# Performance work log

Measured on AMD Instinct MI355X. Metric: run time of the kernel, lower is better.

## Reference

```python
import jax, jax.numpy as jnp
import numpy as np

DK, DV, NH = 512, 256, 8  # matches init_kwargs


def rel_to_abs(x):
    # x: (B, N, L, 2L-1) -> (B, N, L, L) via pad/reshape trick
    B, N, L, _ = x.shape
    x = jnp.pad(x, ((0, 0), (0, 0), (0, 0), (0, 1)))          # (B,N,L,2L)
    x = x.reshape(B, N, L * 2 * L)
    x = jnp.pad(x, ((0, 0), (0, 0), (0, L - 1)))
    x = x.reshape(B, N, L + 1, 2 * L - 1)
    return x[:, :, :L, L - 1:]


def relative_logits_1d(q, rel_k):
    # q: (B, nh, A, Wd, dkh); rel_k: (dkh, 2*Wd-1)
    B, nh, A, Wd, _ = q.shape
    rel = jnp.einsum('bnawc,cm->bnawm', q, rel_k)             # (B,nh,A,Wd,2Wd-1)
    rel = rel.reshape(B, nh * A, Wd, 2 * Wd - 1)
    rel = rel_to_abs(rel).reshape(B, nh, A, 1, Wd, Wd)
    return jnp.broadcast_to(rel, (B, nh, A, A, Wd, Wd))


def reference(x, w_qkv, w_conv, w_out, key_rel_h, key_rel_w):
    B, Cin, H, W = x.shape
    dkh, dvh = DK // NH, DV // NH
    L = H * W
    # 1x1 qkv projection (stride 1)
    qkv = jnp.einsum('bchw,oc->bohw', x, w_qkv)               # (B, 2dk+dv, H, W)
    q = qkv[:, :DK]
    k = qkv[:, DK:2 * DK]
    v = qkv[:, 2 * DK:]
    flat_q = q.reshape(B, NH, dkh, L) * (dkh ** -0.5)
    flat_k = k.reshape(B, NH, dkh, L)
    flat_v = v.reshape(B, NH, dvh, L)
    logits = jnp.einsum('bncs,bnct->bnst', flat_q, flat_k)     # (B,nh,L,L)
    # relative position logits (uses the already-scaled q, as in the torch code)
    qr = flat_q.reshape(B, NH, dkh, H, W).transpose(0, 1, 3, 4, 2)  # (B,nh,H,W,dkh)
    w_rel = relative_logits_1d(qr, key_rel_w)                  # (B,nh,H,H,W,W)
    h_rel = relative_logits_1d(qr.transpose(0, 1, 3, 2, 4), key_rel_h)  # (B,nh,W,W,H,H)
    h_rel = h_rel.transpose(0, 1, 2, 4, 3, 5).reshape(B, NH, L, L)
    w_rel = w_rel.transpose(0, 1, 4, 2, 5, 3).reshape(B, NH, L, L)
    logits = logits + h_rel + w_rel
    weights = jax.nn.softmax(logits, axis=-1)
    attn = jnp.einsum('bnst,bnct->bnsc', weights, flat_v)      # (B,nh,L,dvh)
    attn = attn.transpose(0, 1, 3, 2).reshape(B, DV, H, W)
    attn = jnp.einsum('bchw,oc->bohw', attn, w_out)            # 1x1 out_proj
    conv_out = jax.lax.conv_general_dilated(
        x, w_conv, window_strides=(1, 1), padding=[(1, 1), (1, 1)],
        dimension_numbers=('NCHW', 'OIHW', 'NCHW'))            # (B, out_c-dv, H, W)
    return jnp.concatenate([conv_out, attn], axis=1)


def setup_inputs() -> dict:
    key = jax.random.key(0)
    ks = jax.random.split(key, 6)
    H, W, Cin = 32, 32, 256
    return {
        'x': jax.random.normal(ks[0], (8, Cin, H, W), jnp.float32),
        'w_qkv': jax.random.normal(ks[1], (2 * DK + DV, Cin), jnp.float32) * 0.02,
        'w_conv': jax.random.normal(ks[2], (256, Cin, 3, 3), jnp.float32) * 0.02,
        'w_out': jax.random.normal(ks[3], (DV, DV), jnp.float32) * 0.02,
        'key_rel_h': DK ** -0.5 + jax.random.normal(ks[4], (DK // NH, 2 * H - 1), jnp.float32),
        'key_rel_w': DK ** -0.5 + jax.random.normal(ks[5], (DK // NH, 2 * W - 1), jnp.float32),
    }
```

## Files before the change

kernel.cpp:

```cpp
#include <hip/hip_runtime.h>
#include <cstddef>
#include <cstdint>

#define NB 8
#define CIN 256
#define LL 1024
#define DKC 512
#define DVC 256
#define XPSTRIDE 295936

typedef short short8 __attribute__((ext_vector_type(8)));
typedef float f32x4 __attribute__((ext_vector_type(4)));

__device__ __forceinline__ unsigned short f2bf(float f) {
  unsigned int u = __float_as_uint(f);
  u += 0x7fffu + ((u >> 16) & 1u);
  return (unsigned short)(u >> 16);
}
__device__ __forceinline__ float bf2f(unsigned short u) {
  return __uint_as_float(((unsigned int)u) << 16);
}

__global__ __launch_bounds__(256) void prep_all(
    const float* __restrict__ x, const float* __restrict__ wconv,
    const float* __restrict__ wqkv, const float* __restrict__ wout,
    const float* __restrict__ krh, const float* __restrict__ krw,
    unsigned short* __restrict__ xTp, unsigned short* __restrict__ wtap,
    unsigned short* __restrict__ wqbf, unsigned short* __restrict__ woutbf,
    unsigned short* __restrict__ relTh, unsigned short* __restrict__ relTw) {
  __shared__ float tile[64][65];
  const int bx = blockIdx.x;
  const int tid = threadIdx.x;
  if (bx < 128) {
    const int st = bx & 15;
    const int b = bx >> 4;
    const int s0 = st * 64;
    const int h0 = st * 2;
    for (int cc = 0; cc < 4; ++cc) {
      const int c0 = cc * 64;
      {
        const int row = tid >> 2;
        const int j0 = (tid & 3) * 16;
#pragma unroll
        for (int k = 0; k < 4; ++k)
          *(float4*)&tile[row][j0 + k * 4] =
              *(const float4*)(x + ((size_t)(b * CIN + c0 + row)) * LL + s0 + j0 + k * 4);
      }
      __syncthreads();
      {
        const int sl = tid >> 2;
        const int cb = (tid & 3) * 16;
        unsigned short buf[16];
#pragma unroll
        for (int m = 0; m < 16; ++m) buf[m] = f2bf(tile[cb + m][sl]);
        const int hp = h0 + (sl >> 5) + 1;
        const int wp = (sl & 31) + 1;
        unsigned short* dst = xTp + (size_t)b * XPSTRIDE + (hp * 34 + wp) * 256 + c0 + cb;
        *(uint4*)dst = *(uint4*)&buf[0];
        *(uint4*)(dst + 8) = *(uint4*)&buf[8];
      }
      __syncthreads();
    }
  } else if (bx < 1184) {
    const int idx = (bx - 128) * 256 + tid;
    const int b = idx / 33792;
    const int rem = idx - b * 33792;
    const int pos = rem >> 8, c = rem & 255;
    int hp, wp;
    if (pos < 34) { hp = 0; wp = pos; }
    else if (pos < 68) { hp = 33; wp = pos - 34; }
    else if (pos < 100) { hp = pos - 68 + 1; wp = 0; }
    else { hp = pos - 100 + 1; wp = 33; }
    xTp[(size_t)b * XPSTRIDE + (hp * 34 + wp) * 256 + c] = 0;
  } else {
    const int idx = (bx - 1184) * 256 + tid;
    if (idx < 589824) {
      const int tap = idx >> 16;
      const int rem = idx & 65535;
      wtap[idx] = f2bf(wconv[(size_t)rem * 9 + tap]);
    } else if (idx < 917504) {
      const int j = idx - 589824;
      const int o = j >> 8;
      const float sc = (o < DKC) ? 0.125f * 1.44269504088896f : 1.0f;
      wqbf[j] = f2bf(wqkv[j] * sc);
    } else if (idx < 983040) {
      const int j = idx - 917504;
      woutbf[j] = f2bf(wout[j]);
    } else {
      const int j = idx - 983040;
      const int tbl = j >> 12;
      const int rest = j & 4095;
      const int m = rest >> 6, c = rest & 63;
      const float* src = tbl ? krw : krh;
      unsigned short* dst = tbl ? relTw : relTh;
      const float v = (m < 63) ? src[c * 63 + m] : 0.f;
      dst[m * 64 + c] = f2bf(v);
    }
  }
}

__global__ __launch_bounds__(256) void qkv_mfma(
    const unsigned short* __restrict__ xTp, const unsigned short* __restrict__ wqbf,
    unsigned short* __restrict__ qbf, unsigned short* __restrict__ kbf,
    unsigned short* __restrict__ vbf) {
  __shared__ __align__(16) char smem[16640];
  unsigned short* as = (unsigned short*)smem;
  unsigned short* bs = (unsigned short*)(smem + 8192);
  float (*trans)[65] = (float(*)[65])smem;

  const int tid = threadIdx.x;
  const int lane = tid & 63, w = tid >> 6;
  const int n16 = lane & 15, quad = lane >> 4;
  const int ot = blockIdx.x;
  const int st = blockIdx.y;
  const int b = blockIdx.z;
  const int o0 = ot * 64;
  const int s0 = st * 64;
  const int h0 = st * 2;
  const int trow = tid >> 3, ck = tid & 7;

  const unsigned short* xb = xTp + (size_t)b * XPSTRIDE;
  const unsigned short* wt = wqbf + (size_t)o0 * 256;
  const int wpos = (trow & 31) + 1;

  f32x4 acc[4];
#pragma unroll
  for (int nt = 0; nt < 4; ++nt) acc[nt] = (f32x4){0.f, 0.f, 0.f, 0.f};

  uint4 ra0, ra1, rb0, rb1;
  {
    ra0 = *(const uint4*)(wt + (size_t)trow * 256 + ck * 8);
    ra1 = *(const uint4*)(wt + (size_t)(trow + 32) * 256 + ck * 8);
    rb0 = *(const uint4*)(xb + (size_t)((h0 + 1) * 34 + wpos) * 256 + ck * 8);
    rb1 = *(const uint4*)(xb + (size_t)((h0 + 2) * 34 + wpos) * 256 + ck * 8);
  }
#pragma unroll
  for (int kc = 0; kc < 4; ++kc) {
    __syncthreads();
    *(uint4*)&as[trow * 64 + ((ck ^ (trow & 7)) * 8)] = ra0;
    *(uint4*)&as[(trow + 32) * 64 + ((ck ^ (trow & 7)) * 8)] = ra1;
    *(uint4*)&bs[trow * 64 + ((ck ^ (trow & 7)) * 8)] = rb0;
    *(uint4*)&bs[(trow + 32) * 64 + ((ck ^ (trow & 7)) * 8)] = rb1;
    __syncthreads();
    if (kc < 3) {
      const int c0 = (kc + 1) * 64;
      ra0 = *(const uint4*)(wt + (size_t)trow * 256 + c0 + ck * 8);
      ra1 = *(const uint4*)(wt + (size_t)(trow + 32) * 256 + c0 + ck * 8);
      rb0 = *(const uint4*)(xb + (size_t)((h0 + 1) * 34 + wpos) * 256 + c0 + ck * 8);
      rb1 = *(const uint4*)(xb + (size_t)((h0 + 2) * 34 + wpos) * 256 + c0 + ck * 8);
    }
    short8 a0 = *(const short8*)&as[(w * 16 + n16) * 64 + ((quad ^ (n16 & 7)) * 8)];
    short8 a1 = *(const short8*)&as[(w * 16 + n16) * 64 + (((quad + 4) ^ (n16 & 7)) * 8)];
#pragma unroll
    for (int nt = 0; nt < 4; ++nt) {
      short8 b0 = *(const short8*)&bs[(nt * 16 + n16) * 64 + ((quad ^ (n16 & 7)) * 8)];
      short8 b1 = *(const short8*)&bs[(nt * 16 + n16) * 64 + (((quad + 4) ^ (n16 & 7)) * 8)];
      acc[nt] = __builtin_amdgcn_mfma_f32_16x16x32_bf16(a0, b0, acc[nt], 0, 0, 0);
      acc[nt] = __builtin_amdgcn_mfma_f32_16x16x32_bf16(a1, b1, acc[nt], 0, 0, 0);
    }
  }
  __syncthreads();
#pragma unroll
  for (int nt = 0; nt < 4; ++nt)
#pragma unroll
    for (int reg = 0; reg < 4; ++reg)
      trans[w * 16 + quad * 4 + reg][nt * 16 + n16] = acc[nt][reg];
  __syncthreads();
  const int sl = tid >> 2;
  const int cseg = (tid & 3) * 16;
  unsigned short buf[16];
  if (ot < 16) {
#pragma unroll
    for (int m = 0; m < 16; ++m) buf[m] = f2bf(trans[cseg + m][sl]);
    unsigned short* dst;
    int head;
    if (ot < 8) { dst = qbf; head = ot; }
    else { dst = kbf; head = ot - 8; }
    const size_t base = (((size_t)(b * 8 + head)) * LL + s0 + sl) * 64 + cseg;
    *(uint4*)(dst + base) = *(uint4*)&buf[0];
    *(uint4*)(dst + base + 8) = *(uint4*)&buf[8];
  } else {
#pragma unroll
    for (int m = 0; m < 16; ++m) buf[m] = f2bf(trans[sl][cseg + m]);
    unsigned short* dst = vbf + ((size_t)b * DVC + (ot - 16) * 64 + sl) * LL + s0 + cseg;
    *(uint4*)dst = *(uint4*)&buf[0];
    *(uint4*)(dst + 8) = *(uint4*)&buf[8];
  }
}

__global__ __launch_bounds__(256) void conv_mfma(
    const unsigned short* __restrict__ xTp, const unsigned short* __restrict__ wtap,
    float* __restrict__ out) {
  __shared__ __align__(16) unsigned short as[2][64 * 64];
  __shared__ __align__(16) unsigned short bs[2][64 * 64];
  const int tid = threadIdx.x;
  const int lane = tid & 63, w = tid >> 6;
  const int n16 = lane & 15, quad = lane >> 4;
  const int ot = blockIdx.x;
  const int st = blockIdx.y;
  const int b = blockIdx.z;
  const int s0 = st * 64;
  const int h0 = st * 2;
  const int trow = tid >> 3;
  const int ck = tid & 7;

  const unsigned short* xb = xTp + (size_t)b * XPSTRIDE;
  const unsigned short* wbase = wtap + (size_t)(ot * 64) * 256;

  f32x4 acc[4];
#pragma unroll
  for (int nt = 0; nt < 4; ++nt) acc[nt] = (f32x4){0.f, 0.f, 0.f, 0.f};

  uint4 ra0, ra1, rb0, rb1;
  auto loadtile = [&](int it) {
    const int tap = it >> 2;
    const int c0 = (it & 3) * 64;
    const int dh = tap / 3 - 1;
    const int dw = tap - (tap / 3) * 3 - 1;
    const unsigned short* wt = wbase + (size_t)tap * 65536;
    ra0 = *(const uint4*)(wt + (size_t)trow * 256 + c0 + ck * 8);
    ra1 = *(const uint4*)(wt + (size_t)(trow + 32) * 256 + c0 + ck * 8);
    const int wp = (trow & 31) + dw + 1;
    rb0 = *(const uint4*)(xb + (size_t)((h0 + dh + 1) * 34 + wp) * 256 + c0 + ck * 8);
    rb1 = *(const uint4*)(xb + (size_t)((h0 + dh + 2) * 34 + wp) * 256 + c0 + ck * 8);
  };
  auto stage = [&](int bufi) {
    *(uint4*)&as[bufi][trow * 64 + ((ck ^ (trow & 7)) * 8)] = ra0;
    *(uint4*)&as[bufi][(trow + 32) * 64 + ((ck ^ (trow & 7)) * 8)] = ra1;
    *(uint4*)&bs[bufi][trow * 64 + ((ck ^ (trow & 7)) * 8)] = rb0;
    *(uint4*)&bs[bufi][(trow + 32) * 64 + ((ck ^ (trow & 7)) * 8)] = rb1;
  };
  loadtile(0);
  stage(0);
  for (int it = 0; it < 36; ++it) {
    if (it < 35) loadtile(it + 1);
    __syncthreads();
    const unsigned short* ab = as[it & 1];
    const unsigned short* bb = bs[it & 1];
    short8 a0 = *(const short8*)&ab[(w * 16 + n16) * 64 + ((quad ^ (n16 & 7)) * 8)];
    short8 a1 = *(const short8*)&ab[(w * 16 + n16) * 64 + (((quad + 4) ^ (n16 & 7)) * 8)];
#pragma unroll
    for (int nt = 0; nt < 4; ++nt) {
      short8 b0 = *(const short8*)&bb[(nt * 16 + n16) * 64 + ((quad ^ (n16 & 7)) * 8)];
      short8 b1 = *(const short8*)&bb[(nt * 16 + n16) * 64 + (((quad + 4) ^ (n16 & 7)) * 8)];
      acc[nt] = __builtin_amdgcn_mfma_f32_16x16x32_bf16(a0, b0, acc[nt], 0, 0, 0);
      acc[nt] = __builtin_amdgcn_mfma_f32_16x16x32_bf16(a1, b1, acc[nt], 0, 0, 0);
    }
    if (it < 35) stage((it + 1) & 1);
  }
#pragma unroll
  for (int nt = 0; nt < 4; ++nt)
#pragma unroll
    for (int reg = 0; reg < 4; ++reg)
      out[((size_t)b * 512 + ot * 64 + w * 16 + quad * 4 + reg) * LL + s0 + nt * 16 + n16] =
          acc[nt][reg];
}

__global__ __launch_bounds__(256, 4) void attn_kernel(
    const unsigned short* __restrict__ qbf, const unsigned short* __restrict__ kbf,
    const unsigned short* __restrict__ vbf, const unsigned short* __restrict__ relTh,
    const unsigned short* __restrict__ relTw, unsigned short* __restrict__ abf) {
  __shared__ __align__(16) char smem[28672];
  unsigned short* ks = (unsigned short*)smem;
  unsigned short* vs = (unsigned short*)(smem + 8192);
  unsigned short* ps = (unsigned short*)(smem + 12288);
  unsigned short* rwtT = (unsigned short*)(smem + 20480);
  float* obuf = (float*)smem;

  const int tid = threadIdx.x;
  const int lane = tid & 63, w = tid >> 6;
  const int n16 = lane & 15, quad = lane >> 4;
  const int blk = blockIdx.x;
  const int bn = blk & 63, qb = blk >> 6;
  const int n = bn & 7, b = bn >> 3;
  const int s0 = qb * 64;
  const int aa = 2 * qb + (w >> 1);
  const int pb = (w & 1) * 16;

  const unsigned short* qbase = qbf + ((size_t)(b * 8 + n)) * LL * 64;
  const unsigned short* kbase = kbf + ((size_t)(b * 8 + n)) * LL * 64;
  const unsigned short* vbase = vbf + ((size_t)(b * 8 + n)) * 32 * LL;

  const int ck = tid & 7;
  const int trow = tid >> 3;

  uint4 pk0 = *(const uint4*)(kbase + trow * 64 + ck * 8);
  uint4 pk1 = *(const uint4*)(kbase + (trow + 32) * 64 + ck * 8);
  uint4 pv = *(const uint4*)(vbase + (size_t)trow * LL + ck * 8);

  {
    const int sT = (pb + n16) * 32 + aa;
    short8 ra0 = *(const short8*)(qbase + (size_t)sT * 64 + quad * 8);
    short8 ra1 = *(const short8*)(qbase + (size_t)sT * 64 + 32 + quad * 8);
#pragma unroll
    for (int tbl = 0; tbl < 2; ++tbl) {
      const unsigned short* rel = tbl ? relTh : relTw;
      f32x4 acc[4];
#pragma unroll
      for (int mt = 0; mt < 4; ++mt) acc[mt] = (f32x4){0.f, 0.f, 0.f, 0.f};
#pragma unroll
      for (int mt = 0; mt < 4; ++mt) {
        short8 b0 = *(const short8*)(rel + (mt * 16 + n16) * 64 + quad * 8);
        short8 b1 = *(const short8*)(rel + (mt * 16 + n16) * 64 + 32 + quad * 8);
        acc[mt] = __builtin_amdgcn_mfma_f32_16x16x32_bf16(ra0, b0, acc[mt], 0, 0, 0);
        acc[mt] = __builtin_amdgcn_mfma_f32_16x16x32_bf16(ra1, b1, acc[mt], 0, 0, 0);
      }
      if (tbl == 0) {
#pragma unroll
        for (int mt = 0; mt < 4; ++mt)
#pragma unroll
          for (int reg = 0; reg < 4; ++reg)
            rwtT[(mt * 16 + n16) * 64 +
                 ((w * 16 + quad * 4 + reg) ^ ((n16 & 7) * 8))] = f2bf(acc[mt][reg]);
      } else {
#pragma unroll
        for (int mt = 0; mt < 4; ++mt)
#pragma unroll
          for (int reg = 0; reg < 4; ++reg)
            ps[(w * 16 + quad * 4 + reg) * 64 + mt * 16 + n16] = f2bf(acc[mt][reg]);
      }
    }
  }
  short8 qf0 = *(const short8*)(qbase + (size_t)(s0 + w * 16 + n16) * 64 + quad * 8);
  short8 qf1 = *(const short8*)(qbase + (size_t)(s0 + w * 16 + n16) * 64 + 32 + quad * 8);
  __syncthreads();
  float rhreg[2][4];
#pragma unroll
  for (int tt1 = 0; tt1 < 2; ++tt1)
#pragma unroll
    for (int reg = 0; reg < 4; ++reg) {
      const int iL = quad * 4 + reg;
      rhreg[tt1][reg] = bf2f(ps[(w * 16 + iL) * 64 + tt1 * 16 + n16 + 31 - pb - iL]);
    }

  float lacc[4] = {0.f, 0.f, 0.f, 0.f};
  f32x4 oacc[2];
  oacc[0] = (f32x4){0.f, 0.f, 0.f, 0.f};
  oacc[1] = (f32x4){0.f, 0.f, 0.f, 0.f};

  unsigned short* psw = ps + w * 1024;
  const int rb = w * 16 + quad * 4;

  for (int kt64 = 0; kt64 < 16; ++kt64) {
    const int t0 = kt64 * 64;
    __syncthreads();
    *(uint4*)&ks[trow * 64 + ((ck ^ (trow & 7)) * 8)] = pk0;
    *(uint4*)&ks[(trow + 32) * 64 + ((ck ^ (trow & 7)) * 8)] = pk1;
    *(uint4*)&vs[trow * 64 + ((ck ^ (trow & 7)) * 8)] = pv;
    __syncthreads();
    if (kt64 < 15) {
      const unsigned short* kg = kbase + (size_t)(t0 + 64) * 64;
      pk0 = *(const uint4*)(kg + trow * 64 + ck * 8);
      pk1 = *(const uint4*)(kg + (trow + 32) * 64 + ck * 8);
      pv = *(const uint4*)(vbase + (size_t)trow * LL + t0 + 64 + ck * 8);
    }

    f32x4 sacc[4];
#pragma unroll
    for (int tt = 0; tt < 4; ++tt) sacc[tt] = (f32x4){0.f, 0.f, 0.f, 0.f};
#pragma unroll
    for (int tt = 0; tt < 4; ++tt) {
      short8 kb0 = *(const short8*)&ks[(tt * 16 + n16) * 64 + ((quad ^ (n16 & 7)) * 8)];
      short8 kb1 = *(const short8*)&ks[(tt * 16 + n16) * 64 + (((quad + 4) ^ (n16 & 7)) * 8)];
      sacc[tt] = __builtin_amdgcn_mfma_f32_16x16x32_bf16(qf0, kb0, sacc[tt], 0, 0, 0);
      sacc[tt] = __builtin_amdgcn_mfma_f32_16x16x32_bf16(qf1, kb1, sacc[tt], 0, 0, 0);
    }
    float rwv[2][4];
#pragma unroll
    for (int h = 0; h < 2; ++h) {
      const int mw = (t0 >> 5) + h - aa + 31;
      const ushort4 rw4 = *(const ushort4*)&rwtT[mw * 64 + (rb ^ ((mw & 7) * 8))];
      rwv[h][0] = bf2f(rw4.x); rwv[h][1] = bf2f(rw4.y);
      rwv[h][2] = bf2f(rw4.z); rwv[h][3] = bf2f(rw4.w);
    }
#pragma unroll
    for (int tt = 0; tt < 4; ++tt)
#pragma unroll
      for (int reg = 0; reg < 4; ++reg) {
        const float e =
            __builtin_amdgcn_exp2f(sacc[tt][reg] + rwv[tt >> 1][reg] + rhreg[tt & 1][reg]);
        lacc[reg] += e;
        const int r = quad * 4 + reg;
        psw[r * 64 + (((tt * 2 + (n16 >> 3)) ^ (r & 7)) * 8) + (n16 & 7)] =
            (unsigned short)(__float_as_uint(e) >> 16);
      }
    __asm__ volatile("s_waitcnt lgkmcnt(0)" ::: "memory");
#pragma unroll
    for (int kt = 0; kt < 2; ++kt) {
      short8 pa = *(const short8*)&psw[n16 * 64 + (((quad + 4 * kt) ^ (n16 & 7)) * 8)];
#pragma unroll
      for (int ct = 0; ct < 2; ++ct) {
        short8 vb = *(const short8*)&vs[(ct * 16 + n16) * 64 + (((quad + 4 * kt) ^ (n16 & 7)) * 8)];
        oacc[ct] = __builtin_amdgcn_mfma_f32_16x16x32_bf16(pa, vb, oacc[ct], 0, 0, 0);
      }
    }
  }
  float linv[4];
#pragma unroll
  for (int reg = 0; reg < 4; ++reg) {
    float l = lacc[reg];
#pragma unroll
    for (int m = 1; m < 16; m <<= 1) l += __shfl_xor(l, m, 16);
    linv[reg] = 1.0f / l;
  }
  __syncthreads();
#pragma unroll
  for (int ct = 0; ct < 2; ++ct)
#pragma unroll
    for (int reg = 0; reg < 4; ++reg)
      obuf[(w * 16 + quad * 4 + reg) * 33 + ct * 16 + n16] = oacc[ct][reg] * linv[reg];
  __syncthreads();
  {
    const int row = tid >> 2;
    const int cseg = (tid & 3) * 8;
    unsigned short buf8[8];
#pragma unroll
    for (int m = 0; m < 8; ++m) buf8[m] = f2bf(obuf[row * 33 + cseg + m]);
    *(uint4*)(abf + (((size_t)b * LL) + s0 + row) * 256 + n * 32 + cseg) = *(uint4*)&buf8[0];
  }
}

__global__ __launch_bounds__(256) void proj_mfma(
    const unsigned short* __restrict__ abf, const unsigned short* __restrict__ woutbf,
    float* __restrict__ out) {
  __shared__ __align__(16) unsigned short as[64 * 64];
  __shared__ __align__(16) unsigned short bs[64 * 64];
  const int tid = threadIdx.x;
  const int lane = tid & 63, w = tid >> 6;
  const int n16 = lane & 15, quad = lane >> 4;
  const int ot = blockIdx.x;
  const int st = blockIdx.y;
  const int b = blockIdx.z;
  const int o0 = ot * 64;
  const int s0 = st * 64;
  const int trow = tid >> 3, ck = tid & 7;

  const unsigned short* ab = abf + ((size_t)b * LL + s0) * 256;
  const unsigned short* wt = woutbf + (size_t)o0 * 256;

  f32x4 acc[4];
#pragma unroll
  for (int nt = 0; nt < 4; ++nt) acc[nt] = (f32x4){0.f, 0.f, 0.f, 0.f};

  uint4 ra0, ra1, rb0, rb1;
  ra0 = *(const uint4*)(wt + (size_t)trow * 256 + ck * 8);
  ra1 = *(const uint4*)(wt + (size_t)(trow + 32) * 256 + ck * 8);
  rb0 = *(const uint4*)(ab + (size_t)trow * 256 + ck * 8);
  rb1 = *(const uint4*)(ab + (size_t)(trow + 32) * 256 + ck * 8);
#pragma unroll
  for (int kc = 0; kc < 4; ++kc) {
    __syncthreads();
    *(uint4*)&as[trow * 64 + ((ck ^ (trow & 7)) * 8)] = ra0;
    *(uint4*)&as[(trow + 32) * 64 + ((ck ^ (trow & 7)) * 8)] = ra1;
    *(uint4*)&bs[trow * 64 + ((ck ^ (trow & 7)) * 8)] = rb0;
    *(uint4*)&bs[(trow + 32) * 64 + ((ck ^ (trow & 7)) * 8)] = rb1;
    __syncthreads();
    if (kc < 3) {
      const int c0 = (kc + 1) * 64;
      ra0 = *(const uint4*)(wt + (size_t)trow * 256 + c0 + ck * 8);
      ra1 = *(const uint4*)(wt + (size_t)(trow + 32) * 256 + c0 + ck * 8);
      rb0 = *(const uint4*)(ab + (size_t)trow * 256 + c0 + ck * 8);
      rb1 = *(const uint4*)(ab + (size_t)(trow + 32) * 256 + c0 + ck * 8);
    }
    short8 a0 = *(const short8*)&as[(w * 16 + n16) * 64 + ((quad ^ (n16 & 7)) * 8)];
    short8 a1 = *(const short8*)&as[(w * 16 + n16) * 64 + (((quad + 4) ^ (n16 & 7)) * 8)];
#pragma unroll
    for (int nt = 0; nt < 4; ++nt) {
      short8 b0 = *(const short8*)&bs[(nt * 16 + n16) * 64 + ((quad ^ (n16 & 7)) * 8)];
      short8 b1 = *(const short8*)&bs[(nt * 16 + n16) * 64 + (((quad + 4) ^ (n16 & 7)) * 8)];
      acc[nt] = __builtin_amdgcn_mfma_f32_16x16x32_bf16(a0, b0, acc[nt], 0, 0, 0);
      acc[nt] = __builtin_amdgcn_mfma_f32_16x16x32_bf16(a1, b1, acc[nt], 0, 0, 0);
    }
  }
#pragma unroll
  for (int nt = 0; nt < 4; ++nt)
#pragma unroll
    for (int reg = 0; reg < 4; ++reg)
      out[((size_t)b * 512 + 256 + o0 + w * 16 + quad * 4 + reg) * LL + s0 + nt * 16 + n16] =
          acc[nt][reg];
}

extern "C" void kernel_launch(void* const* d_in, const int* in_sizes, int n_in,
                              void* d_out, int out_size, void* d_ws, size_t ws_size,
                              hipStream_t stream) {
  const float* x     = (const float*)d_in[0];
  const float* wqkv  = (const float*)d_in[1];
  const float* wconv = (const float*)d_in[2];
  const float* wout  = (const float*)d_in[3];
  const float* krh   = (const float*)d_in[4];
  const float* krw   = (const float*)d_in[5];
  float* out = (float*)d_out;

  unsigned short* qbf = (unsigned short*)d_ws;
  unsigned short* kbf = qbf + (size_t)NB * 8 * LL * 64;
  unsigned short* vbf = kbf + (size_t)NB * 8 * LL * 64;
  unsigned short* abf = vbf + (size_t)NB * DVC * LL;
  unsigned short* relTh = abf + (size_t)NB * LL * DVC;
  unsigned short* relTw = relTh + 4096;
  unsigned short* xTp = relTw + 4096;
  unsigned short* wtap = xTp + (size_t)NB * XPSTRIDE;
  unsigned short* wqbf = wtap + 589824;
  unsigned short* woutbf = wqbf + 327680;

  prep_all<<<dim3(5056), 256, 0, stream>>>(x, wconv, wqkv, wout, krh, krw,
                                           xTp, wtap, wqbf, woutbf, relTh, relTw);
  qkv_mfma<<<dim3(20, 16, NB), 256, 0, stream>>>(xTp, wqbf, qbf, kbf, vbf);
  conv_mfma<<<dim3(4, 16, NB), 256, 0, stream>>>(xTp, wtap, out);
  attn_kernel<<<dim3(1024), 256, 0, stream>>>(qbf, kbf, vbf, relTh, relTw, abf);
  proj_mfma<<<dim3(4, 16, NB), 256, 0, stream>>>(abf, woutbf, out);
}
```

Baseline: 154.0 us.

## Double-buffer K/V tiles in attention and halve conv spatial tile

The attention kernel now double-buffers its K/V shared-memory tiles. The next tile is written into the alternate buffer after the PV MFMAs, which removes one of the two block barriers per key tile. The conv kernel's spatial tile shrinks from 64 to 32 positions (one image row), doubling the grid to improve occupancy on the many CUs. Shared memory per attention block grows to about 40KB, which may lower occupancy, and the rwtT write skips the unused 64th row.

```diff
diff --git a/kernel.cpp b/kernel.cpp
--- a/kernel.cpp
+++ b/kernel.cpp
@@ -192,26 +192,25 @@
     const unsigned short* __restrict__ xTp, const unsigned short* __restrict__ wtap,
     float* __restrict__ out) {
   __shared__ __align__(16) unsigned short as[2][64 * 64];
-  __shared__ __align__(16) unsigned short bs[2][64 * 64];
+  __shared__ __align__(16) unsigned short bs[2][32 * 64];
   const int tid = threadIdx.x;
   const int lane = tid & 63, w = tid >> 6;
   const int n16 = lane & 15, quad = lane >> 4;
   const int ot = blockIdx.x;
   const int st = blockIdx.y;
   const int b = blockIdx.z;
-  const int s0 = st * 64;
-  const int h0 = st * 2;
+  const int s0 = st * 32;
   const int trow = tid >> 3;
   const int ck = tid & 7;
 
   const unsigned short* xb = xTp + (size_t)b * XPSTRIDE;
   const unsigned short* wbase = wtap + (size_t)(ot * 64) * 256;
 
-  f32x4 acc[4];
-#pragma unroll
-  for (int nt = 0; nt < 4; ++nt) acc[nt] = (f32x4){0.f, 0.f, 0.f, 0.f};
-
-  uint4 ra0, ra1, rb0, rb1;
+  f32x4 acc[2];
+#pragma unroll
+  for (int nt = 0; nt < 2; ++nt) acc[nt] = (f32x4){0.f, 0.f, 0.f, 0.f};
+
+  uint4 ra0, ra1, rb0;
   auto loadtile = [&](int it) {
     const int tap = it >> 2;
     const int c0 = (it & 3) * 64;
@@ -220,15 +219,13 @@
     const unsigned short* wt = wbase + (size_t)tap * 65536;
     ra0 = *(const uint4*)(wt + (size_t)trow * 256 + c0 + ck * 8);
     ra1 = *(const uint4*)(wt + (size_t)(trow + 32) * 256 + c0 + ck * 8);
-    const int wp = (trow & 31) + dw + 1;
-    rb0 = *(const uint4*)(xb + (size_t)((h0 + dh + 1) * 34 + wp) * 256 + c0 + ck * 8);
-    rb1 = *(const uint4*)(xb + (size_t)((h0 + dh + 2) * 34 + wp) * 256 + c0 + ck * 8);
+    const int wp = trow + dw + 1;
+    rb0 = *(const uint4*)(xb + (size_t)((st + dh + 1) * 34 + wp) * 256 + c0 + ck * 8);
   };
   auto stage = [&](int bufi) {
     *(uint4*)&as[bufi][trow * 64 + ((ck ^ (trow & 7)) * 8)] = ra0;
     *(uint4*)&as[bufi][(trow + 32) * 64 + ((ck ^ (trow & 7)) * 8)] = ra1;
     *(uint4*)&bs[bufi][trow * 64 + ((ck ^ (trow & 7)) * 8)] = rb0;
-    *(uint4*)&bs[bufi][(trow + 32) * 64 + ((ck ^ (trow & 7)) * 8)] = rb1;
   };
   loadtile(0);
   stage(0);
@@ -240,7 +237,7 @@
     short8 a0 = *(const short8*)&ab[(w * 16 + n16) * 64 + ((quad ^ (n16 & 7)) * 8)];
     short8 a1 = *(const short8*)&ab[(w * 16 + n16) * 64 + (((quad + 4) ^ (n16 & 7)) * 8)];
 #pragma unroll
-    for (int nt = 0; nt < 4; ++nt) {
+    for (int nt = 0; nt < 2; ++nt) {
       short8 b0 = *(const short8*)&bb[(nt * 16 + n16) * 64 + ((quad ^ (n16 & 7)) * 8)];
       short8 b1 = *(const short8*)&bb[(nt * 16 + n16) * 64 + (((quad + 4) ^ (n16 & 7)) * 8)];
       acc[nt] = __builtin_amdgcn_mfma_f32_16x16x32_bf16(a0, b0, acc[nt], 0, 0, 0);
@@ -249,7 +246,7 @@
     if (it < 35) stage((it + 1) & 1);
   }
 #pragma unroll
-  for (int nt = 0; nt < 4; ++nt)
+  for (int nt = 0; nt < 2; ++nt)
 #pragma unroll
     for (int reg = 0; reg < 4; ++reg)
       out[((size_t)b * 512 + ot * 64 + w * 16 + quad * 4 + reg) * LL + s0 + nt * 16 + n16] =
@@ -260,11 +257,11 @@
     const unsigned short* __restrict__ qbf, const unsigned short* __restrict__ kbf,
     const unsigned short* __restrict__ vbf, const unsigned short* __restrict__ relTh,
     const unsigned short* __restrict__ relTw, unsigned short* __restrict__ abf) {
-  __shared__ __align__(16) char smem[28672];
+  __shared__ __align__(16) char smem[40832];
   unsigned short* ks = (unsigned short*)smem;
-  unsigned short* vs = (unsigned short*)(smem + 8192);
-  unsigned short* ps = (unsigned short*)(smem + 12288);
-  unsigned short* rwtT = (unsigned short*)(smem + 20480);
+  unsigned short* vs = (unsigned short*)(smem + 16384);
+  unsigned short* ps = (unsigned short*)(smem + 24576);
+  unsigned short* rwtT = (unsigned short*)(smem + 32768);
   float* obuf = (float*)smem;
 
   const int tid = threadIdx.x;
@@ -306,12 +303,15 @@
         acc[mt] = __builtin_amdgcn_mfma_f32_16x16x32_bf16(ra1, b1, acc[mt], 0, 0, 0);
       }
       if (tbl == 0) {
-#pragma unroll
-        for (int mt = 0; mt < 4; ++mt)
-#pragma unroll
-          for (int reg = 0; reg < 4; ++reg)
-            rwtT[(mt * 16 + n16) * 64 +
-                 ((w * 16 + quad * 4 + reg) ^ ((n16 & 7) * 8))] = f2bf(acc[mt][reg]);
+        if ((3 * 16 + n16) < 63 || n16 < 15) {
+#pragma unroll
+          for (int mt = 0; mt < 4; ++mt)
+            if (mt * 16 + n16 < 63)
+#pragma unroll
+              for (int reg = 0; reg < 4; ++reg)
+                rwtT[(mt * 16 + n16) * 64 +
+                     ((w * 16 + quad * 4 + reg) ^ ((n16 & 7) * 8))] = f2bf(acc[mt][reg]);
+        }
       } else {
 #pragma unroll
         for (int mt = 0; mt < 4; ++mt)
@@ -323,6 +323,11 @@
   }
   short8 qf0 = *(const short8*)(qbase + (size_t)(s0 + w * 16 + n16) * 64 + quad * 8);
   short8 qf1 = *(const short8*)(qbase + (size_t)(s0 + w * 16 + n16) * 64 + 32 + quad * 8);
+  {
+    *(uint4*)&ks[trow * 64 + ((ck ^ (trow & 7)) * 8)] = pk0;
+    *(uint4*)&ks[(trow + 32) * 64 + ((ck ^ (trow & 7)) * 8)] = pk1;
+    *(uint4*)&vs[trow * 64 + ((ck ^ (trow & 7)) * 8)] = pv;
+  }
   __syncthreads();
   float rhreg[2][4];
 #pragma unroll
@@ -341,27 +346,26 @@
   unsigned short* psw = ps + w * 1024;
   const int rb = w * 16 + quad * 4;
 
+  int cur = 0;
   for (int kt64 = 0; kt64 < 16; ++kt64) {
     const int t0 = kt64 * 64;
-    __syncthreads();
-    *(uint4*)&ks[trow * 64 + ((ck ^ (trow & 7)) * 8)] = pk0;
-    *(uint4*)&ks[(trow + 32) * 64 + ((ck ^ (trow & 7)) * 8)] = pk1;
-    *(uint4*)&vs[trow * 64 + ((ck ^ (trow & 7)) * 8)] = pv;
-    __syncthreads();
     if (kt64 < 15) {
       const unsigned short* kg = kbase + (size_t)(t0 + 64) * 64;
       pk0 = *(const uint4*)(kg + trow * 64 + ck * 8);
       pk1 = *(const uint4*)(kg + (trow + 32) * 64 + ck * 8);
       pv = *(const uint4*)(vbase + (size_t)trow * LL + t0 + 64 + ck * 8);
     }
+    __syncthreads();
+    const unsigned short* ksb = ks + cur * 4096;
+    const unsigned short* vsb = vs + cur * 2048;
 
     f32x4 sacc[4];
 #pragma unroll
     for (int tt = 0; tt < 4; ++tt) sacc[tt] = (f32x4){0.f, 0.f, 0.f, 0.f};
 #pragma unroll
     for (int tt = 0; tt < 4; ++tt) {
-      short8 kb0 = *(const short8*)&ks[(tt * 16 + n16) * 64 + ((quad ^ (n16 & 7)) * 8)];
-      short8 kb1 = *(const short8*)&ks[(tt * 16 + n16) * 64 + (((quad + 4) ^ (n16 & 7)) * 8)];
+      short8 kb0 = *(const short8*)&ksb[(tt * 16 + n16) * 64 + ((quad ^ (n16 & 7)) * 8)];
+      short8 kb1 = *(const short8*)&ksb[(tt * 16 + n16) * 64 + (((quad + 4) ^ (n16 & 7)) * 8)];
       sacc[tt] = __builtin_amdgcn_mfma_f32_16x16x32_bf16(qf0, kb0, sacc[tt], 0, 0, 0);
       sacc[tt] = __builtin_amdgcn_mfma_f32_16x16x32_bf16(qf1, kb1, sacc[tt], 0, 0, 0);
     }
@@ -390,10 +394,18 @@
       short8 pa = *(const short8*)&psw[n16 * 64 + (((quad + 4 * kt) ^ (n16 & 7)) * 8)];
 #pragma unroll
       for (int ct = 0; ct < 2; ++ct) {
-        short8 vb = *(const short8*)&vs[(ct * 16 + n16) * 64 + (((quad + 4 * kt) ^ (n16 & 7)) * 8)];
+        short8 vb = *(const short8*)&vsb[(ct * 16 + n16) * 64 + (((quad + 4 * kt) ^ (n16 & 7)) * 8)];
         oacc[ct] = __builtin_amdgcn_mfma_f32_16x16x32_bf16(pa, vb, oacc[ct], 0, 0, 0);
       }
     }
+    if (kt64 < 15) {
+      unsigned short* kd = ks + (cur ^ 1) * 4096;
+      unsigned short* vd = vs + (cur ^ 1) * 2048;
+      *(uint4*)&kd[trow * 64 + ((ck ^ (trow & 7)) * 8)] = pk0;
+      *(uint4*)&kd[(trow + 32) * 64 + ((ck ^ (trow & 7)) * 8)] = pk1;
+      *(uint4*)&vd[trow * 64 + ((ck ^ (trow & 7)) * 8)] = pv;
+    }
+    cur ^= 1;
   }
   float linv[4];
 #pragma unroll
@@ -505,7 +517,7 @@
   prep_all<<<dim3(5056), 256, 0, stream>>>(x, wconv, wqkv, wout, krh, krw,
                                            xTp, wtap, wqbf, woutbf, relTh, relTw);
   qkv_mfma<<<dim3(20, 16, NB), 256, 0, stream>>>(xTp, wqbf, qbf, kbf, vbf);
-  conv_mfma<<<dim3(4, 16, NB), 256, 0, stream>>>(xTp, wtap, out);
+  conv_mfma<<<dim3(4, 32, NB), 256, 0, stream>>>(xTp, wtap, out);
   attn_kernel<<<dim3(1024), 256, 0, stream>>>(qbf, kbf, vbf, relTh, relTw, abf);
   proj_mfma<<<dim3(4, 16, NB), 256, 0, stream>>>(abf, woutbf, out);
 }
```

Result: slower. 158.9 us (+3.2%).
